# Kernel optimization log

Hardware: AMD Instinct MI355X
Metric: run time of the kernel (lower is better)

The kernel has to match this reference:

```python
import jax, jax.numpy as jnp
import numpy as np
from jax import lax

B, NL, W = 1024, 64, 2048
EPS_N = 1e-8   # added to n in m12 denominator (as in torch source)
EPS_Y = 1e-9   # added to E before admittance division (as in torch source)


def setup_inputs() -> dict:
    key = jax.random.key(0)
    k1, k2 = jax.random.split(key)
    # refractive indices of typical dielectrics, thicknesses ~quarter-wave in nm
    n_layers = 1.0 + 1.5 * jax.random.uniform(k1, (B, NL), dtype=jnp.float32)
    d_layers = 20.0 + 200.0 * jax.random.uniform(k2, (B, NL), dtype=jnp.float32)
    wavelengths = jnp.linspace(400.0, 800.0, W, dtype=jnp.float32)
    return {"n_layers": n_layers, "d_layers": d_layers, "wavelengths": wavelengths}


def reference(n_layers, d_layers, wavelengths):
    # n_layers: (B, N) real -> complex64; d_layers: (B, N) nm; wavelengths: (W,) nm
    n = n_layers.astype(jnp.complex64)
    k0 = (2.0 * np.pi / wavelengths).astype(jnp.complex64)  # (W,)
    num_layers = n.shape[1]

    def step(M, nd):
        # M: (B, W, 2, 2) complex64 running product; nd = (n_i, d_i) each (B,)
        n_i, d_i = nd
        phi = n_i[:, None] * d_i[:, None] * k0[None, :]          # (B, W)
        c = jnp.cos(phi)
        s = jnp.sin(phi)
        m12 = -1j * s / (n_i[:, None] + EPS_N)
        m21 = -1j * n_i[:, None] * s
        # layer characteristic matrix (B, W, 2, 2)
        M_layer = jnp.stack(
            [jnp.stack([c, m12], axis=-1), jnp.stack([m21, c], axis=-1)],
            axis=-2,
        )
        M_new = jnp.einsum("bwij,bwjk->bwik", M, M_layer)
        return M_new, None

    M0 = jnp.broadcast_to(
        jnp.eye(2, dtype=jnp.complex64), (n.shape[0], k0.shape[0], 2, 2)
    )
    # scan over interior layers 1 .. N-2 (substrate/ambient are semi-infinite)
    xs = (n[:, 1 : num_layers - 1].T, d_layers[:, 1 : num_layers - 1].T)
    M, _ = lax.scan(step, M0, xs)

    n_in = n[:, 0]    # (B,) incident-side index
    n_sub = n[:, -1]  # (B,) substrate index
    # EH = M @ [1, n_sub]^T  ->  E, H : (B, W)
    E = M[..., 0, 0] + M[..., 0, 1] * n_sub[:, None]
    H = M[..., 1, 0] + M[..., 1, 1] * n_sub[:, None]
    Y = H / (E + EPS_Y)
    r = (n_in[:, None] - Y) / (n_in[:, None] + Y)
    R = jnp.abs(r) ** 2
    return R.astype(jnp.float32)
```

## Files before the change

### kernel.cpp

```cpp
#include <hip/hip_runtime.h>
#include <math.h>

constexpr int B  = 1024;
constexpr int NL = 64;
constexpr int W  = 2048;
constexpr int INNER = NL - 2;
constexpr float EPS_N = 1e-8f;
constexpr float EPS_Y = 1e-9f;

typedef float v2f __attribute__((ext_vector_type(2)));

__global__ __launch_bounds__(256)
void tmm_kernel(const float* __restrict__ n_layers,
                const float* __restrict__ d_layers,
                const float* __restrict__ wavelengths,
                float* __restrict__ out)
{
    __shared__ float4 s_layer[INNER];
    __shared__ float s_edge[2];

    const int b   = blockIdx.y;
    const int tid = threadIdx.x;
    const int w   = blockIdx.x * 256 + tid;

    if (tid < INNER) {
        const float n = n_layers[b * NL + 1 + tid];
        const float d = d_layers[b * NL + 1 + tid];
        s_layer[tid] = make_float4(n * d, n, -n, 1.0f / (n + EPS_N));
    }
    if (tid == INNER) {
        s_edge[0] = n_layers[b * NL];
        s_edge[1] = n_layers[b * NL + NL - 1];
    }
    __syncthreads();

    const float inv_lambda = 1.0f / wavelengths[w];

    v2f p = {1.0f, 0.0f};
    v2f q = {0.0f, 1.0f};

    #pragma unroll
    for (int i = 0; i < INNER; ++i) {
        const float4 L = s_layer[i];
        const float phi_rev = L.x * inv_lambda;
        const float s = __builtin_amdgcn_sinf(phi_rev);
        const float c = __builtin_amdgcn_cosf(phi_rev);

        const v2f nn  = {L.y, L.z};
        const v2f ss  = {s, s};
        const v2f ns2 = nn * ss;
        const float is = L.w * s;
        const v2f is2 = {-is, is};
        const v2f c2  = {c, c};

        const v2f pold = p;
        p = __builtin_elementwise_fma(q,    ns2, p * c2);
        q = __builtin_elementwise_fma(pold, is2, q * c2);
    }

    const float a  = p.x;
    const float cc = p.y;
    const float bb = q.x;
    const float dd = q.y;

    const float n_in  = s_edge[0];
    const float n_sub = s_edge[1];

    const float Er = a + EPS_Y;
    const float Ei = bb * n_sub;
    const float Hr = dd * n_sub;
    const float Hi = cc;

    const float Nr = fmaf(n_in, Er, -Hr);
    const float Ni = fmaf(n_in, Ei, -Hi);
    const float Dr = fmaf(n_in, Er,  Hr);
    const float Di = fmaf(n_in, Ei,  Hi);

    const float R = (Nr * Nr + Ni * Ni) / (Dr * Dr + Di * Di);
    out[b * W + w] = R;
}

extern "C" void kernel_launch(void* const* d_in, const int* in_sizes, int n_in,
                              void* d_out, int out_size, void* d_ws, size_t ws_size,
                              hipStream_t stream)
{
    const float* n_layers    = (const float*)d_in[0];
    const float* d_layers    = (const float*)d_in[1];
    const float* wavelengths = (const float*)d_in[2];
    float* out = (float*)d_out;

    dim3 grid(W / 256, B);
    dim3 block(256);
    tmm_kernel<<<grid, block, 0, stream>>>(n_layers, d_layers, wavelengths, out);
}
```

Baseline: 104.7 us.

## Process two wavelengths per thread with packed matrix-entry updates

Each thread now computes two adjacent wavelengths. The packed float2 lanes hold the two wavelengths instead of two matrix entries, so the per-layer update becomes four fully packed FMAs with no shuffling of (-is, is) vectors. Each layer's shared-memory load is shared across two wavelengths, and the output and wavelength accesses are vectorised to float2. The grid halves. The cost is more registers per thread and half as many blocks, and the transcendental count per output is unchanged.

```diff
diff --git a/kernel.cpp b/kernel.cpp
--- a/kernel.cpp
+++ b/kernel.cpp
@@ -16,17 +16,20 @@
                 const float* __restrict__ wavelengths,
                 float* __restrict__ out)
 {
-    __shared__ float4 s_layer[INNER];
-    __shared__ float s_edge[2];
+    __shared__ float4 s_layer[INNER][2];
+    __shared__ float  s_edge[2];
 
     const int b   = blockIdx.y;
     const int tid = threadIdx.x;
-    const int w   = blockIdx.x * 256 + tid;
+    const int w0  = blockIdx.x * 512 + tid * 2;
 
     if (tid < INNER) {
-        const float n = n_layers[b * NL + 1 + tid];
-        const float d = d_layers[b * NL + 1 + tid];
-        s_layer[tid] = make_float4(n * d, n, -n, 1.0f / (n + EPS_N));
+        const float n  = n_layers[b * NL + 1 + tid];
+        const float d  = d_layers[b * NL + 1 + tid];
+        const float nd = n * d;
+        const float rc = 1.0f / (n + EPS_N);
+        s_layer[tid][0] = make_float4(nd, nd, n, n);
+        s_layer[tid][1] = make_float4(rc, rc, 0.0f, 0.0f);
     }
     if (tid == INNER) {
         s_edge[0] = n_layers[b * NL];
@@ -34,50 +37,66 @@
     }
     __syncthreads();
 
-    const float inv_lambda = 1.0f / wavelengths[w];
+    const float2 wl  = *(const float2*)&wavelengths[w0];
+    const v2f invl = { 1.0f / wl.x, 1.0f / wl.y };
 
-    v2f p = {1.0f, 0.0f};
-    v2f q = {0.0f, 1.0f};
+    v2f av = {1.0f, 1.0f};
+    v2f bv = {0.0f, 0.0f};
+    v2f cv = {0.0f, 0.0f};
+    v2f dv = {1.0f, 1.0f};
 
     #pragma unroll
     for (int i = 0; i < INNER; ++i) {
-        const float4 L = s_layer[i];
-        const float phi_rev = L.x * inv_lambda;
-        const float s = __builtin_amdgcn_sinf(phi_rev);
-        const float c = __builtin_amdgcn_cosf(phi_rev);
+        const float4 A  = s_layer[i][0];
+        const float2 Rr = *(const float2*)&s_layer[i][1];
+        const v2f nd2 = {A.x, A.y};
+        const v2f nn2 = {A.z, A.w};
+        const v2f rr2 = {Rr.x, Rr.y};
 
-        const v2f nn  = {L.y, L.z};
-        const v2f ss  = {s, s};
-        const v2f ns2 = nn * ss;
-        const float is = L.w * s;
-        const v2f is2 = {-is, is};
-        const v2f c2  = {c, c};
+        const v2f ph = nd2 * invl;
+        v2f s2, c2;
+        s2.x = __builtin_amdgcn_sinf(ph.x);
+        s2.y = __builtin_amdgcn_sinf(ph.y);
+        c2.x = __builtin_amdgcn_cosf(ph.x);
+        c2.y = __builtin_amdgcn_cosf(ph.y);
 
-        const v2f pold = p;
-        p = __builtin_elementwise_fma(q,    ns2, p * c2);
-        q = __builtin_elementwise_fma(pold, is2, q * c2);
+        const v2f ns2 = nn2 * s2;
+        const v2f sn2 = rr2 * s2;
+
+        const v2f an = __builtin_elementwise_fma(bv,  ns2, av * c2);
+        const v2f bn = __builtin_elementwise_fma(-av, sn2, bv * c2);
+        const v2f cn = __builtin_elementwise_fma(-dv, ns2, cv * c2);
+        const v2f dn = __builtin_elementwise_fma(cv,  sn2, dv * c2);
+        av = an; bv = bn; cv = cn; dv = dn;
     }
-
-    const float a  = p.x;
-    const float cc = p.y;
-    const float bb = q.x;
-    const float dd = q.y;
 
     const float n_in  = s_edge[0];
     const float n_sub = s_edge[1];
 
-    const float Er = a + EPS_Y;
-    const float Ei = bb * n_sub;
-    const float Hr = dd * n_sub;
-    const float Hi = cc;
-
-    const float Nr = fmaf(n_in, Er, -Hr);
-    const float Ni = fmaf(n_in, Ei, -Hi);
-    const float Dr = fmaf(n_in, Er,  Hr);
-    const float Di = fmaf(n_in, Ei,  Hi);
-
-    const float R = (Nr * Nr + Ni * Ni) / (Dr * Dr + Di * Di);
-    out[b * W + w] = R;
+    float2 Rout;
+    {
+        const float Er = av.x + EPS_Y;
+        const float Ei = bv.x * n_sub;
+        const float Hr = dv.x * n_sub;
+        const float Hi = cv.x;
+        const float Nr = fmaf(n_in, Er, -Hr);
+        const float Ni = fmaf(n_in, Ei, -Hi);
+        const float Dr = fmaf(n_in, Er,  Hr);
+        const float Di = fmaf(n_in, Ei,  Hi);
+        Rout.x = (Nr * Nr + Ni * Ni) / (Dr * Dr + Di * Di);
+    }
+    {
+        const float Er = av.y + EPS_Y;
+        const float Ei = bv.y * n_sub;
+        const float Hr = dv.y * n_sub;
+        const float Hi = cv.y;
+        const float Nr = fmaf(n_in, Er, -Hr);
+        const float Ni = fmaf(n_in, Ei, -Hi);
+        const float Dr = fmaf(n_in, Er,  Hr);
+        const float Di = fmaf(n_in, Ei,  Hi);
+        Rout.y = (Nr * Nr + Ni * Ni) / (Dr * Dr + Di * Di);
+    }
+    *(float2*)&out[b * W + w0] = Rout;
 }
 
 extern "C" void kernel_launch(void* const* d_in, const int* in_sizes, int n_in,
@@ -89,7 +108,7 @@
     const float* wavelengths = (const float*)d_in[2];
     float* out = (float*)d_out;
 
-    dim3 grid(W / 256, B);
+    dim3 grid(W / 512, B);
     dim3 block(256);
     tmm_kernel<<<grid, block, 0, stream>>>(n_layers, d_layers, wavelengths, out);
 }
```

Measured after the change: 93.96 us. 10.3% less time.

## Compute four wavelengths per thread with scalar FMAs and vectorized I/O

Applied to the files above, without the earlier changes.

Each thread now handles four consecutive wavelengths, so every shared-memory layer read is reused four times and loads and stores become float4. The grid shrinks by four in x, giving fewer blocks and less per-block setup. The packed v2f math is replaced by scalar FMAs, and launch bounds now ask for 8 blocks per SM. The trade-offs are higher register pressure and fewer threads in flight. The kernel is dominated by sin/cos transcendentals, so the overall gain may be limited.

```diff
diff --git a/kernel.cpp b/kernel.cpp
--- a/kernel.cpp
+++ b/kernel.cpp
@@ -8,25 +8,23 @@
 constexpr float EPS_N = 1e-8f;
 constexpr float EPS_Y = 1e-9f;
 
-typedef float v2f __attribute__((ext_vector_type(2)));
-
-__global__ __launch_bounds__(256)
+__global__ __launch_bounds__(256, 8)
 void tmm_kernel(const float* __restrict__ n_layers,
                 const float* __restrict__ d_layers,
                 const float* __restrict__ wavelengths,
                 float* __restrict__ out)
 {
     __shared__ float4 s_layer[INNER];
-    __shared__ float s_edge[2];
+    __shared__ float  s_edge[2];
 
     const int b   = blockIdx.y;
     const int tid = threadIdx.x;
-    const int w   = blockIdx.x * 256 + tid;
+    const int w0  = blockIdx.x * 1024 + tid * 4;
 
     if (tid < INNER) {
         const float n = n_layers[b * NL + 1 + tid];
         const float d = d_layers[b * NL + 1 + tid];
-        s_layer[tid] = make_float4(n * d, n, -n, 1.0f / (n + EPS_N));
+        s_layer[tid] = make_float4(n * d, n, 1.0f / (n + EPS_N), 0.0f);
     }
     if (tid == INNER) {
         s_edge[0] = n_layers[b * NL];
@@ -34,50 +32,48 @@
     }
     __syncthreads();
 
-    const float inv_lambda = 1.0f / wavelengths[w];
+    const float4 wl = *(const float4*)&wavelengths[w0];
+    float il[4] = { 1.0f / wl.x, 1.0f / wl.y, 1.0f / wl.z, 1.0f / wl.w };
 
-    v2f p = {1.0f, 0.0f};
-    v2f q = {0.0f, 1.0f};
+    float a[4]  = {1.0f, 1.0f, 1.0f, 1.0f};
+    float bm[4] = {0.0f, 0.0f, 0.0f, 0.0f};
+    float cm[4] = {0.0f, 0.0f, 0.0f, 0.0f};
+    float d[4]  = {1.0f, 1.0f, 1.0f, 1.0f};
 
     #pragma unroll
     for (int i = 0; i < INNER; ++i) {
         const float4 L = s_layer[i];
-        const float phi_rev = L.x * inv_lambda;
-        const float s = __builtin_amdgcn_sinf(phi_rev);
-        const float c = __builtin_amdgcn_cosf(phi_rev);
+        #pragma unroll
+        for (int k = 0; k < 4; ++k) {
+            const float ph = L.x * il[k];
+            const float s  = __builtin_amdgcn_sinf(ph);
+            const float c  = __builtin_amdgcn_cosf(ph);
+            const float ns = L.y * s;
+            const float sn = L.z * s;
 
-        const v2f nn  = {L.y, L.z};
-        const v2f ss  = {s, s};
-        const v2f ns2 = nn * ss;
-        const float is = L.w * s;
-        const v2f is2 = {-is, is};
-        const v2f c2  = {c, c};
-
-        const v2f pold = p;
-        p = __builtin_elementwise_fma(q,    ns2, p * c2);
-        q = __builtin_elementwise_fma(pold, is2, q * c2);
+            const float an = fmaf(bm[k],  ns, a[k]  * c);
+            const float bn = fmaf(a[k],  -sn, bm[k] * c);
+            const float cn = fmaf(d[k],  -ns, cm[k] * c);
+            const float dn = fmaf(cm[k],  sn, d[k]  * c);
+            a[k] = an; bm[k] = bn; cm[k] = cn; d[k] = dn;
+        }
     }
-
-    const float a  = p.x;
-    const float cc = p.y;
-    const float bb = q.x;
-    const float dd = q.y;
 
     const float n_in  = s_edge[0];
     const float n_sub = s_edge[1];
 
-    const float Er = a + EPS_Y;
-    const float Ei = bb * n_sub;
-    const float Hr = dd * n_sub;
-    const float Hi = cc;
-
-    const float Nr = fmaf(n_in, Er, -Hr);
-    const float Ni = fmaf(n_in, Ei, -Hi);
-    const float Dr = fmaf(n_in, Er,  Hr);
-    const float Di = fmaf(n_in, Ei,  Hi);
-
-    const float R = (Nr * Nr + Ni * Ni) / (Dr * Dr + Di * Di);
-    out[b * W + w] = R;
+    float r[4];
+    #pragma unroll
+    for (int k = 0; k < 4; ++k) {
+        const float Er = a[k] + EPS_Y;
+        const float Ei = bm[k] * n_sub;
+        const float Hr = d[k] * n_sub;
+        const float Hi = cm[k];
+        const float Nr = fmaf(n_in, Er, -Hr), Ni = fmaf(n_in, Ei, -Hi);
+        const float Dr = fmaf(n_in, Er,  Hr), Di = fmaf(n_in, Ei,  Hi);
+        r[k] = (Nr * Nr + Ni * Ni) / (Dr * Dr + Di * Di);
+    }
+    *(float4*)&out[b * W + w0] = make_float4(r[0], r[1], r[2], r[3]);
 }
 
 extern "C" void kernel_launch(void* const* d_in, const int* in_sizes, int n_in,
@@ -89,7 +85,7 @@
     const float* wavelengths = (const float*)d_in[2];
     float* out = (float*)d_out;
 
-    dim3 grid(W / 256, B);
+    dim3 grid(W / 1024, B);
     dim3 block(256);
     tmm_kernel<<<grid, block, 0, stream>>>(n_layers, d_layers, wavelengths, out);
 }
```

Result: no change. 102.9 us (-1.8%).
